# Kernel optimization log

Hardware: AMD Instinct MI355X
Metric: run time of the kernel (lower is better)

## Reference

```python
import jax, jax.numpy as jnp
import numpy as np

EPS = 1e-08  # smooth in CELoss


def _lovasz_grad(fg_sorted):
    # Alg. 1 of the Lovasz-Softmax paper; fg_sorted: [P] floats in {0,1}
    gts = fg_sorted.sum()
    intersection = gts - jnp.cumsum(fg_sorted)
    union = gts + jnp.cumsum(1.0 - fg_sorted)
    jaccard = 1.0 - intersection / union
    # first-difference: jaccard[1:] - jaccard[:-1], keep jaccard[0]
    return jnp.concatenate([jaccard[:1], jaccard[1:] - jaccard[:-1]])


def setup_inputs() -> dict:
    key = jax.random.key(0)
    k1, k2 = jax.random.split(key)
    B, C, D, H, W = 1, 3, 96, 256, 256
    probas = jax.random.normal(k1, (B, C, D, H, W), dtype=jnp.float32)
    cls = jax.random.randint(k2, (B, D, H, W), 0, C)
    # one-hot label volume [B, C, D, H, W], matching labels[0][c] == 1 usage
    labels = jax.nn.one_hot(cls, C, axis=1, dtype=jnp.int32)
    weight = jnp.ones((C,), dtype=jnp.float32)  # weight=[1,1,1]
    return {"probas": probas, "weight": weight, "labels": labels}


def reference(probas, weight, labels):
    C = probas.shape[1]
    # flatten_probas (dim==5 path): softmax over classes, flatten to [P, C]
    p = jax.nn.softmax(probas, axis=1)
    p = jnp.moveaxis(p, 1, -1).reshape(-1, C)
    # label reconstruction: 0*ch0 + 1*ch1 + 2*ch2 from one-hot channels
    lab = (labels[0, 1] + 2 * labels[0, 2]).reshape(-1)  # [P] int class ids

    total = jnp.zeros((), dtype=p.dtype)
    count = jnp.zeros((), dtype=p.dtype)
    for c in range(C):
        fg = (lab == c).astype(p.dtype)              # [P]
        present = fg.sum() > 0                       # classes='present'
        # CELoss(softmax=False, average='None'): -fg * log(pred + eps)
        errors = -fg * jnp.log(p[:, c] + EPS)        # [P]
        order = jnp.argsort(-errors)                 # descending sort perm
        errors_sorted = errors[order]
        fg_sorted = fg[order]
        g = jax.lax.stop_gradient(_lovasz_grad(fg_sorted))
        loss_c = weight[c] * jnp.dot(errors_sorted, g)
        total = total + jnp.where(present, loss_c, 0.0)
        count = count + jnp.where(present, 1.0, 0.0)
    # mean over present classes (empty -> 0)
    return jnp.where(count > 0, total / jnp.maximum(count, 1.0), 0.0)
```

## Files before the change

kernel.cpp:

```cpp
#include <hip/hip_runtime.h>


#define EPS 1e-8f

__device__ __forceinline__ void px_acc(float za, float zb, float zc, int la, int lb,
                                       float& s0, float& s1, float& s2,
                                       float& n0, float& n1, float& n2)
{
    int lab = la + 2 * lb;
    float m  = fmaxf(za, fmaxf(zb, zc));
    float ea = __expf(za - m);
    float eb = __expf(zb - m);
    float ec = __expf(zc - m);
    float denom = ea + eb + ec;
    float e = (lab == 0) ? ea : ((lab == 1) ? eb : ec);
    float p = e / denom;
    float err = -__logf(p + EPS);
    float f0 = (lab == 0) ? 1.f : 0.f;
    float f1 = (lab == 1) ? 1.f : 0.f;
    float f2 = (lab == 2) ? 1.f : 0.f;
    s0 += f0 * err;  s1 += f1 * err;  s2 += f2 * err;
    n0 += f0;        n1 += f1;        n2 += f2;
}

__global__ __launch_bounds__(256) void lovasz_reduce_kernel(
    const float* __restrict__ probas,
    const int*   __restrict__ labels,
    float* __restrict__ partial,
    int P4, int P, int nblocks)
{
    const float4* z0 = (const float4*)(probas);
    const float4* z1 = (const float4*)(probas + (size_t)P);
    const float4* z2 = (const float4*)(probas + 2 * (size_t)P);
    const int4*   l1 = (const int4*)(labels + (size_t)P);
    const int4*   l2 = (const int4*)(labels + 2 * (size_t)P);

    float s0 = 0.f, s1 = 0.f, s2 = 0.f;
    float n0 = 0.f, n1 = 0.f, n2 = 0.f;

    const int base = blockIdx.x * 1024 + threadIdx.x;
    #pragma unroll
    for (int j = 0; j < 4; ++j) {
        int i = base + j * 256;
        if (i < P4) {
            float4 a = z0[i], b = z1[i], c = z2[i];
            int4   u = l1[i], v = l2[i];
            px_acc(a.x, b.x, c.x, u.x, v.x, s0, s1, s2, n0, n1, n2);
            px_acc(a.y, b.y, c.y, u.y, v.y, s0, s1, s2, n0, n1, n2);
            px_acc(a.z, b.z, c.z, u.z, v.z, s0, s1, s2, n0, n1, n2);
            px_acc(a.w, b.w, c.w, u.w, v.w, s0, s1, s2, n0, n1, n2);
        }
    }

    #pragma unroll
    for (int off = 32; off > 0; off >>= 1) {
        s0 += __shfl_down(s0, off);
        s1 += __shfl_down(s1, off);
        s2 += __shfl_down(s2, off);
        n0 += __shfl_down(n0, off);
        n1 += __shfl_down(n1, off);
        n2 += __shfl_down(n2, off);
    }

    __shared__ float red[6][4];
    int wave = threadIdx.x >> 6;
    int lane = threadIdx.x & 63;
    if (lane == 0) {
        red[0][wave] = s0; red[1][wave] = s1; red[2][wave] = s2;
        red[3][wave] = n0; red[4][wave] = n1; red[5][wave] = n2;
    }
    __syncthreads();
    if (threadIdx.x < 6) {
        int k = threadIdx.x;
        partial[(size_t)k * nblocks + blockIdx.x] =
            red[k][0] + red[k][1] + red[k][2] + red[k][3];
    }
}

__global__ __launch_bounds__(256) void lovasz_finalize_kernel(
    const float* __restrict__ partial, int nblocks,
    const float* __restrict__ probas, const int* __restrict__ labels,
    const float* __restrict__ weight, float* __restrict__ out,
    int P4, int P)
{
    float acc[6] = {0.f, 0.f, 0.f, 0.f, 0.f, 0.f};
    for (int b = threadIdx.x; b < nblocks; b += 256) {
        #pragma unroll
        for (int k = 0; k < 6; ++k)
            acc[k] += partial[(size_t)k * nblocks + b];
    }

    #pragma unroll
    for (int k = 0; k < 6; ++k)
        #pragma unroll
        for (int off = 32; off > 0; off >>= 1)
            acc[k] += __shfl_down(acc[k], off);

    __shared__ float red[6][4];
    int wave = threadIdx.x >> 6;
    int lane = threadIdx.x & 63;
    if (lane == 0) {
        #pragma unroll
        for (int k = 0; k < 6; ++k) red[k][wave] = acc[k];
    }
    __syncthreads();
    if (threadIdx.x == 0) {
        float s[6];
        #pragma unroll
        for (int k = 0; k < 6; ++k)
            s[k] = red[k][0] + red[k][1] + red[k][2] + red[k][3];
        for (int i = 4 * P4; i < P; ++i) {
            px_acc(probas[i], probas[(size_t)P + i], probas[2 * (size_t)P + i],
                   labels[(size_t)P + i], labels[2 * (size_t)P + i],
                   s[0], s[1], s[2], s[3], s[4], s[5]);
        }
        float total = 0.f, cnt = 0.f;
        #pragma unroll
        for (int c = 0; c < 3; ++c) {
            if (s[3 + c] > 0.f) {
                total += weight[c] * s[c] / s[3 + c];
                cnt += 1.f;
            }
        }
        out[0] = (cnt > 0.f) ? total / cnt : 0.f;
    }
}

extern "C" void kernel_launch(void* const* d_in, const int* in_sizes, int n_in,
                              void* d_out, int out_size, void* d_ws, size_t ws_size,
                              hipStream_t stream) {
    const float* probas = (const float*)d_in[0];
    const float* weight = (const float*)d_in[1];
    const int*   labels = (const int*)d_in[2];
    float* partial = (float*)d_ws;

    int total = in_sizes[0];
    int P  = total / 3;
    int P4 = P / 4;
    int nblocks = (P4 + 1023) / 1024;

    lovasz_reduce_kernel<<<nblocks, 256, 0, stream>>>(probas, labels, partial,
                                                      P4, P, nblocks);
    lovasz_finalize_kernel<<<1, 256, 0, stream>>>(partial, nblocks, probas,
                                                  labels, weight, (float*)d_out,
                                                  P4, P);
}
```

Measured before the change: 166.9 us.

## Use persistent grid-stride reduction with register double-buffered loads

```diff
diff --git a/kernel.cpp b/kernel.cpp
--- a/kernel.cpp
+++ b/kernel.cpp
@@ -2,6 +2,7 @@
 
 
 #define EPS 1e-8f
+#define BLK 256
 
 __device__ __forceinline__ void px_acc(float za, float zb, float zc, int la, int lb,
                                        float& s0, float& s1, float& s2,
@@ -23,11 +24,22 @@
     n0 += f0;        n1 += f1;        n2 += f2;
 }
 
-__global__ __launch_bounds__(256) void lovasz_reduce_kernel(
+__device__ __forceinline__ void px4(const float4& a, const float4& b, const float4& c,
+                                    const int4& u, const int4& v,
+                                    float& s0, float& s1, float& s2,
+                                    float& n0, float& n1, float& n2)
+{
+    px_acc(a.x, b.x, c.x, u.x, v.x, s0, s1, s2, n0, n1, n2);
+    px_acc(a.y, b.y, c.y, u.y, v.y, s0, s1, s2, n0, n1, n2);
+    px_acc(a.z, b.z, c.z, u.z, v.z, s0, s1, s2, n0, n1, n2);
+    px_acc(a.w, b.w, c.w, u.w, v.w, s0, s1, s2, n0, n1, n2);
+}
+
+__global__ __launch_bounds__(BLK) void lovasz_reduce_kernel(
     const float* __restrict__ probas,
     const int*   __restrict__ labels,
     float* __restrict__ partial,
-    int P4, int P, int nblocks)
+    int P4, int P, int niter, int nblocks)
 {
     const float4* z0 = (const float4*)(probas);
     const float4* z1 = (const float4*)(probas + (size_t)P);
@@ -38,17 +50,30 @@
     float s0 = 0.f, s1 = 0.f, s2 = 0.f;
     float n0 = 0.f, n1 = 0.f, n2 = 0.f;
 
-    const int base = blockIdx.x * 1024 + threadIdx.x;
-    #pragma unroll
-    for (int j = 0; j < 4; ++j) {
-        int i = base + j * 256;
+    const int tid    = blockIdx.x * BLK + threadIdx.x;
+    const int stride = nblocks * BLK;
+
+    if (niter > 0) {
+        int i = tid;
+        float4 a0 = z0[i], b0 = z1[i], c0 = z2[i];
+        int4   u0 = l1[i], v0 = l2[i];
+        for (int it = 1; it < niter; ++it) {
+            int inext = i + stride;
+            float4 a1 = z0[inext], b1 = z1[inext], c1 = z2[inext];
+            int4   u1 = l1[inext], v1 = l2[inext];
+            px4(a0, b0, c0, u0, v0, s0, s1, s2, n0, n1, n2);
+            a0 = a1; b0 = b1; c0 = c1; u0 = u1; v0 = v1;
+            i = inext;
+        }
+        px4(a0, b0, c0, u0, v0, s0, s1, s2, n0, n1, n2);
+    }
+
+    {
+        int i = niter * stride + tid;
         if (i < P4) {
             float4 a = z0[i], b = z1[i], c = z2[i];
             int4   u = l1[i], v = l2[i];
-            px_acc(a.x, b.x, c.x, u.x, v.x, s0, s1, s2, n0, n1, n2);
-            px_acc(a.y, b.y, c.y, u.y, v.y, s0, s1, s2, n0, n1, n2);
-            px_acc(a.z, b.z, c.z, u.z, v.z, s0, s1, s2, n0, n1, n2);
-            px_acc(a.w, b.w, c.w, u.w, v.w, s0, s1, s2, n0, n1, n2);
+            px4(a, b, c, u, v, s0, s1, s2, n0, n1, n2);
         }
     }
 
@@ -137,10 +162,13 @@
     int total = in_sizes[0];
     int P  = total / 3;
     int P4 = P / 4;
-    int nblocks = (P4 + 1023) / 1024;
 
-    lovasz_reduce_kernel<<<nblocks, 256, 0, stream>>>(probas, labels, partial,
-                                                      P4, P, nblocks);
+    const int nblocks = 2048;
+    int stride = nblocks * BLK;
+    int niter  = P4 / stride;
+
+    lovasz_reduce_kernel<<<nblocks, BLK, 0, stream>>>(probas, labels, partial,
+                                                      P4, P, niter, nblocks);
     lovasz_finalize_kernel<<<1, 256, 0, stream>>>(partial, nblocks, probas,
                                                   labels, weight, (float*)d_out,
                                                   P4, P);
```

Result: no change. 165.9 us (-0.6%).
